# Kernel optimization log

Hardware: AMD Instinct MI355X
Metric: run time of the kernel (lower is better)

## Reference

```python
import jax, jax.numpy as jnp
import numpy as np

B, C, H, W = 4, 150, 384, 512  # C = cfg.MODEL.DECODER_OUTPUT_C


def setup_inputs() -> dict:
    key = jax.random.key(0)
    k1, k2, k3, k4, k5 = jax.random.split(key, 5)
    pred_logit = jax.random.normal(k1, (B, C, H, W), dtype=jnp.float32)
    gt_bins = jax.random.randint(k2, (B, 1, H, W), 0, C)  # int bin index per pixel
    gt = jax.random.uniform(k3, (B, 1, H, W), dtype=jnp.float32)  # unused by the loss math
    mask = (jax.random.uniform(k4, (B, 1, H, W)) > 0.5).astype(jnp.float32)  # binary 0/1 mask
    # cfg.DATASET.WCE_LOSS_WEIGHT, row-normalized as in __init__
    w = jax.random.uniform(k5, (C, C), dtype=jnp.float32) + 0.1
    weight = w / jnp.sum(w, axis=1, keepdims=True)
    return {"pred_logit": pred_logit, "gt_bins": gt_bins, "gt": gt,
            "mask": mask, "weight": weight}


def reference(pred_logit, gt_bins, gt, mask, weight):
    # region == 'out_range': mask used as-is
    Cn = pred_logit.shape[1]
    # log_softmax over channel dim, then flatten to [N, C] with rows ordered (b,h,w)
    lp = jax.nn.log_softmax(pred_logit, axis=1)            # [B,C,H,W]
    lp = jnp.moveaxis(lp, 1, -1).reshape(-1, Cn)           # [N,C]
    m = mask.reshape(-1, 1)                                # [N,1]
    lp = lp * m                                            # mask log-preds
    # one_hot(gt_bins) * mask @ weight  ==  row-gather of weight, masked
    per_class_w = weight[gt_bins.reshape(-1)] * m          # [N,C]
    valid_pixels = jnp.sum(m > 0.0).astype(lp.dtype)
    loss = -jnp.sum(per_class_w * lp) / valid_pixels
    return loss
```

## Files before the change

kernel.cpp:

```cpp
#include <hip/hip_runtime.h>
#include <hip/hip_fp16.h>

namespace {
constexpr int C    = 150;
constexpr int HW   = 384 * 512;
constexpr int NPIX = 4 * HW;
constexpr long CHW = (long)C * HW;
constexpr int TPB  = 256;
constexpr int PPT  = 4;
constexpr int NBLK = NPIX / (TPB * PPT);
constexpr int WSTR = 154;
}

__global__ __launch_bounds__(TPB) void wcel_main(
    const float* __restrict__ pred,
    const int*   __restrict__ gtb,
    const float* __restrict__ mask,
    const float* __restrict__ weight,
    float* __restrict__ acc)
{
    __shared__ __half wlds[C * WSTR];
    __shared__ float rn[TPB / 64], rv[TPB / 64];

    for (int i = threadIdx.x; i < C * C; i += TPB) {
        int row = i / C;
        int col = i - row * C;
        wlds[row * WSTR + col] = __float2half(weight[i]);
    }
    __syncthreads();

    int p = (blockIdx.x * TPB + threadIdx.x) * PPT;
    int b = p / HW;
    int r = p - b * HW;
    const float* base = pred + (size_t)b * CHW + r;

    float4 m4 = *(const float4*)(mask + p);
    int4   g4 = *(const int4*)(gtb + p);
    const __half2* w0 = (const __half2*)(wlds + g4.x * WSTR);
    const __half2* w1 = (const __half2*)(wlds + g4.y * WSTR);
    const __half2* w2 = (const __half2*)(wlds + g4.z * WSTR);
    const __half2* w3 = (const __half2*)(wlds + g4.w * WSTR);

    float s0 = 0.f, s1 = 0.f, s2 = 0.f, s3 = 0.f;
    float d0 = 0.f, d1 = 0.f, d2 = 0.f, d3 = 0.f;

    #pragma unroll 5
    for (int cp = 0; cp < C / 2; ++cp) {
        float4 xa = *(const float4*)(base + (size_t)(2 * cp) * HW);
        float4 xb = *(const float4*)(base + (size_t)(2 * cp + 1) * HW);
        float2 v0 = __half22float2(w0[cp]);
        float2 v1 = __half22float2(w1[cp]);
        float2 v2 = __half22float2(w2[cp]);
        float2 v3 = __half22float2(w3[cp]);

        d0 = fmaf(v0.x, xa.x, d0); d0 = fmaf(v0.y, xb.x, d0);
        d1 = fmaf(v1.x, xa.y, d1); d1 = fmaf(v1.y, xb.y, d1);
        d2 = fmaf(v2.x, xa.z, d2); d2 = fmaf(v2.y, xb.z, d2);
        d3 = fmaf(v3.x, xa.w, d3); d3 = fmaf(v3.y, xb.w, d3);

        s0 += __expf(xa.x); s0 += __expf(xb.x);
        s1 += __expf(xa.y); s1 += __expf(xb.y);
        s2 += __expf(xa.z); s2 += __expf(xb.z);
        s3 += __expf(xa.w); s3 += __expf(xb.w);
    }

    float num = m4.x * (__logf(s0) - d0) + m4.y * (__logf(s1) - d1)
              + m4.z * (__logf(s2) - d2) + m4.w * (__logf(s3) - d3);
    float val = m4.x + m4.y + m4.z + m4.w;

    #pragma unroll
    for (int off = 32; off > 0; off >>= 1) {
        num += __shfl_down(num, off);
        val += __shfl_down(val, off);
    }
    int lane = threadIdx.x & 63, wid = threadIdx.x >> 6;
    if (lane == 0) { rn[wid] = num; rv[wid] = val; }
    __syncthreads();
    if (threadIdx.x == 0) {
        float n = 0.f, v = 0.f;
        #pragma unroll
        for (int i = 0; i < TPB / 64; ++i) { n += rn[i]; v += rv[i]; }
        atomicAdd(&acc[0], n);
        atomicAdd(&acc[1], v);
    }
}

__global__ void wcel_final(const float* __restrict__ acc, float* __restrict__ out)
{
    out[0] = acc[0] / acc[1];
}

extern "C" void kernel_launch(void* const* d_in, const int* in_sizes, int n_in,
                              void* d_out, int out_size, void* d_ws, size_t ws_size,
                              hipStream_t stream)
{
    const float* pred   = (const float*)d_in[0];
    const int*   gtb    = (const int*)  d_in[1];
    const float* mask   = (const float*)d_in[3];
    const float* weight = (const float*)d_in[4];
    float* acc = (float*)d_ws;

    hipMemsetAsync(acc, 0, 2 * sizeof(float), stream);
    wcel_main<<<NBLK, TPB, 0, stream>>>(pred, gtb, mask, weight, acc);
    wcel_final<<<1, 1, 0, stream>>>(acc, (float*)d_out);
}
```

Measured before the change: 615.8 us.

## Use 512-thread blocks with two pixels per thread and deterministic partial reduction

Each block now has 512 threads, and each thread handles 2 pixels instead of 4. The per-pixel dot and exp sums are split into two independent accumulators to shorten dependency chains. The global atomicAdds and the memset are replaced by per-block partials, which a 256-thread final kernel reduces. Bigger blocks spread the cost of staging the weight table in LDS over more pixels and may raise occupancy. In exchange, loads shrink from float4 to float2 per channel row, which may lower memory efficiency.

```diff
diff --git a/kernel.cpp b/kernel.cpp
--- a/kernel.cpp
+++ b/kernel.cpp
@@ -6,18 +6,18 @@
 constexpr int HW   = 384 * 512;
 constexpr int NPIX = 4 * HW;
 constexpr long CHW = (long)C * HW;
-constexpr int TPB  = 256;
-constexpr int PPT  = 4;
+constexpr int TPB  = 512;
+constexpr int PPT  = 2;
 constexpr int NBLK = NPIX / (TPB * PPT);
 constexpr int WSTR = 154;
 }
 
-__global__ __launch_bounds__(TPB) void wcel_main(
+__global__ __launch_bounds__(TPB, 6) void wcel_main(
     const float* __restrict__ pred,
     const int*   __restrict__ gtb,
     const float* __restrict__ mask,
     const float* __restrict__ weight,
-    float* __restrict__ acc)
+    float* __restrict__ part)
 {
     __shared__ __half wlds[C * WSTR];
     __shared__ float rn[TPB / 64], rv[TPB / 64];
@@ -34,39 +34,31 @@
     int r = p - b * HW;
     const float* base = pred + (size_t)b * CHW + r;
 
-    float4 m4 = *(const float4*)(mask + p);
-    int4   g4 = *(const int4*)(gtb + p);
-    const __half2* w0 = (const __half2*)(wlds + g4.x * WSTR);
-    const __half2* w1 = (const __half2*)(wlds + g4.y * WSTR);
-    const __half2* w2 = (const __half2*)(wlds + g4.z * WSTR);
-    const __half2* w3 = (const __half2*)(wlds + g4.w * WSTR);
+    float2 m2 = *(const float2*)(mask + p);
+    int2   g2 = *(const int2*)(gtb + p);
+    const __half2* w0 = (const __half2*)(wlds + g2.x * WSTR);
+    const __half2* w1 = (const __half2*)(wlds + g2.y * WSTR);
 
-    float s0 = 0.f, s1 = 0.f, s2 = 0.f, s3 = 0.f;
-    float d0 = 0.f, d1 = 0.f, d2 = 0.f, d3 = 0.f;
+    float sa0 = 0.f, sb0 = 0.f, sa1 = 0.f, sb1 = 0.f;
+    float da0 = 0.f, db0 = 0.f, da1 = 0.f, db1 = 0.f;
 
     #pragma unroll 5
     for (int cp = 0; cp < C / 2; ++cp) {
-        float4 xa = *(const float4*)(base + (size_t)(2 * cp) * HW);
-        float4 xb = *(const float4*)(base + (size_t)(2 * cp + 1) * HW);
+        float2 xa = *(const float2*)(base + (size_t)(2 * cp) * HW);
+        float2 xb = *(const float2*)(base + (size_t)(2 * cp + 1) * HW);
         float2 v0 = __half22float2(w0[cp]);
         float2 v1 = __half22float2(w1[cp]);
-        float2 v2 = __half22float2(w2[cp]);
-        float2 v3 = __half22float2(w3[cp]);
 
-        d0 = fmaf(v0.x, xa.x, d0); d0 = fmaf(v0.y, xb.x, d0);
-        d1 = fmaf(v1.x, xa.y, d1); d1 = fmaf(v1.y, xb.y, d1);
-        d2 = fmaf(v2.x, xa.z, d2); d2 = fmaf(v2.y, xb.z, d2);
-        d3 = fmaf(v3.x, xa.w, d3); d3 = fmaf(v3.y, xb.w, d3);
+        da0 = fmaf(v0.x, xa.x, da0); db0 = fmaf(v0.y, xb.x, db0);
+        da1 = fmaf(v1.x, xa.y, da1); db1 = fmaf(v1.y, xb.y, db1);
 
-        s0 += __expf(xa.x); s0 += __expf(xb.x);
-        s1 += __expf(xa.y); s1 += __expf(xb.y);
-        s2 += __expf(xa.z); s2 += __expf(xb.z);
-        s3 += __expf(xa.w); s3 += __expf(xb.w);
+        sa0 += __expf(xa.x); sb0 += __expf(xb.x);
+        sa1 += __expf(xa.y); sb1 += __expf(xb.y);
     }
 
-    float num = m4.x * (__logf(s0) - d0) + m4.y * (__logf(s1) - d1)
-              + m4.z * (__logf(s2) - d2) + m4.w * (__logf(s3) - d3);
-    float val = m4.x + m4.y + m4.z + m4.w;
+    float num = m2.x * (__logf(sa0 + sb0) - (da0 + db0))
+              + m2.y * (__logf(sa1 + sb1) - (da1 + db1));
+    float val = m2.x + m2.y;
 
     #pragma unroll
     for (int off = 32; off > 0; off >>= 1) {
@@ -80,14 +72,34 @@
         float n = 0.f, v = 0.f;
         #pragma unroll
         for (int i = 0; i < TPB / 64; ++i) { n += rn[i]; v += rv[i]; }
-        atomicAdd(&acc[0], n);
-        atomicAdd(&acc[1], v);
+        part[2 * blockIdx.x]     = n;
+        part[2 * blockIdx.x + 1] = v;
     }
 }
 
-__global__ void wcel_final(const float* __restrict__ acc, float* __restrict__ out)
+__global__ __launch_bounds__(256) void wcel_final(const float* __restrict__ part,
+                                                  float* __restrict__ out)
 {
-    out[0] = acc[0] / acc[1];
+    __shared__ float rn[4], rv[4];
+    float n = 0.f, v = 0.f;
+    #pragma unroll
+    for (int k = 0; k < NBLK / 256; ++k) {
+        float2 pv = ((const float2*)part)[threadIdx.x + k * 256];
+        n += pv.x; v += pv.y;
+    }
+    #pragma unroll
+    for (int off = 32; off > 0; off >>= 1) {
+        n += __shfl_down(n, off);
+        v += __shfl_down(v, off);
+    }
+    int lane = threadIdx.x & 63, wid = threadIdx.x >> 6;
+    if (lane == 0) { rn[wid] = n; rv[wid] = v; }
+    __syncthreads();
+    if (threadIdx.x == 0) {
+        float nn = rn[0] + rn[1] + rn[2] + rn[3];
+        float vv = rv[0] + rv[1] + rv[2] + rv[3];
+        out[0] = nn / vv;
+    }
 }
 
 extern "C" void kernel_launch(void* const* d_in, const int* in_sizes, int n_in,
@@ -98,9 +110,8 @@
     const int*   gtb    = (const int*)  d_in[1];
     const float* mask   = (const float*)d_in[3];
     const float* weight = (const float*)d_in[4];
-    float* acc = (float*)d_ws;
+    float* part = (float*)d_ws;
 
-    hipMemsetAsync(acc, 0, 2 * sizeof(float), stream);
-    wcel_main<<<NBLK, TPB, 0, stream>>>(pred, gtb, mask, weight, acc);
-    wcel_final<<<1, 1, 0, stream>>>(acc, (float*)d_out);
+    wcel_main<<<NBLK, TPB, 0, stream>>>(pred, gtb, mask, weight, part);
+    wcel_final<<<1, 256, 0, stream>>>(part, (float*)d_out);
 }
```

After: 606.6 us. No clear change (-1.5%).
